# Performance work log

Measured on AMD Instinct MI355X. Metric: run time of the kernel, lower is better.

## Reference

```python
import jax, jax.numpy as jnp
import numpy as np

B, N, F, S = 32, 512, 101, 10   # batch, set size, str_fea_len, expansion_size
E, H, L = 128, 4, 3             # embed_dim, num_heads, n_encoders
EH = E * H
TAB = 100                       # atom-feature table rows


def _ln(x, g, b, eps=1e-5):
    m = jnp.mean(x, -1, keepdims=True)
    v = jnp.var(x, -1, keepdims=True)
    return (x - m) / jnp.sqrt(v + eps) * g + b


def setup_inputs() -> dict:
    key = jax.random.key(0)
    ks = iter(jax.random.split(key, 48))
    nrm = lambda shape: jax.random.normal(next(ks), shape, jnp.float32) * 0.05
    return {
        'str_fea': jax.random.uniform(next(ks), (B, N, F), jnp.float32),
        'comp_fea': jax.random.randint(next(ks), (B, N), 0, TAB),
        'cell_fea': jax.random.normal(next(ks), (B, 6), jnp.float32),
        'af_table': jax.random.uniform(next(ks), (TAB, 92), jnp.float32),
        'comp_w': nrm((92, E)), 'comp_b': jnp.zeros((E,), jnp.float32),
        'emb_w': nrm(((F - 1) * S, E)), 'emb_b': jnp.zeros((E,), jnp.float32),
        'ln_g': jnp.ones((L, E), jnp.float32), 'ln_b': jnp.zeros((L, E), jnp.float32),
        'wq': nrm((L, E, EH)), 'bq': jnp.zeros((L, EH), jnp.float32),
        'wk': nrm((L, E, EH)), 'bk': jnp.zeros((L, EH), jnp.float32),
        'wv': nrm((L, E, EH)), 'bv': jnp.zeros((L, EH), jnp.float32),
        'inproj_w': nrm((L, EH, 3 * EH)), 'inproj_b': jnp.zeros((L, 3 * EH), jnp.float32),
        'out_w': nrm((L, EH, E)), 'out_b': jnp.zeros((L, E), jnp.float32),
        'ffn_w': nrm((L, E, E)), 'ffn_b': jnp.zeros((L, E), jnp.float32),
        'ln2_g': jnp.ones((E,), jnp.float32), 'ln2_b': jnp.zeros((E,), jnp.float32),
        'final_w': nrm((E, 1)), 'final_b': jnp.zeros((1,), jnp.float32),
    }


def reference(str_fea, comp_fea, cell_fea, af_table, comp_w, comp_b, emb_w, emb_b,
              ln_g, ln_b, wq, bq, wk, bk, wv, bv, inproj_w, inproj_b,
              out_w, out_b, ffn_w, ffn_b, ln2_g, ln2_b, final_w, final_b):
    weights = str_fea[:, :, 0:1]                                  # [B,N,1]
    # AtomFeaturizer + composition embedding
    comp = af_table[comp_fea] @ comp_w + comp_b                   # [B,N,E]
    # DistanceExpansion: (1 - (d - i/S))**2 for i in 0..S-1
    d = str_fea[:, :, 1:]                                         # [B,N,F-1]
    starter = jnp.arange(S, dtype=str_fea.dtype) / S
    de = (1.0 - (d[..., None] - starter)) ** 2                    # [B,N,F-1,S]
    de = de.reshape(d.shape[0], d.shape[1], (F - 1) * S)
    strf = de @ emb_w + emb_b                                     # [B,N,E]
    x = comp + strf
    x_init = x
    mask = jnp.sum(weights, -1) == 0.0                            # [B,N] key padding
    w_row = weights[..., 0]                                       # [B,N]
    hd = EH // H
    scale = 1.0 / np.sqrt(hd)
    for l in range(L):
        xn = _ln(x, ln_g[l], ln_b[l])
        qin = xn @ wq[l] + bq[l]                                  # [B,N,EH]
        kin = xn @ wk[l] + bk[l]
        vin = xn @ wv[l] + bv[l]                                  # used as V in manual attention
        # torch.nn.MultiheadAttention in-projection (v-block unused: att_output discarded)
        q = qin @ inproj_w[l][:, :EH] + inproj_b[l][:EH]
        k = kin @ inproj_w[l][:, EH:2 * EH] + inproj_b[l][EH:2 * EH]
        qh = q.reshape(q.shape[0], q.shape[1], H, hd)
        kh = k.reshape(k.shape[0], k.shape[1], H, hd)
        logits = jnp.einsum('bihd,bjhd->bhij', qh, kh) * scale    # [B,H,N,N]
        logits = jnp.where(mask[:, None, None, :], -1e9, logits)
        attn = jnp.mean(jax.nn.softmax(logits, -1), axis=1)       # head-averaged [B,N,N]
        # external edge-weight masking + renormalization
        aw = attn * w_row[:, None, :]
        aw = aw / jnp.sum(aw, -1, keepdims=True)
        att_out = jnp.einsum('bij,bjd->bid', aw, vin)             # [B,N,EH]
        o1 = x + att_out @ out_w[l] + out_b[l]
        o2 = jax.nn.softplus(_ln(o1, ln_g[l], ln_b[l]) @ ffn_w[l] + ffn_b[l])
        x = _ln(o1 + o2, ln_g[l], ln_b[l])
    x = jnp.sum(weights * (x + x_init), axis=1)                   # weighted pool [B,E]
    x = _ln(x, ln2_g, ln2_b)
    return x @ final_w + final_b                                  # [B,1]
```

## Files before the change

### kernel.cpp

```cpp
#include <hip/hip_runtime.h>
#include <math.h>

#define B_ 32
#define N_ 512
#define F_ 101
#define E_ 128
#define H_ 4
#define EH_ 512
#define L_ 3
#define M_ (B_*N_)

typedef __attribute__((ext_vector_type(8))) short s8v;
typedef __attribute__((ext_vector_type(8))) unsigned short us8v;
typedef __attribute__((ext_vector_type(4))) float f4v;
typedef __attribute__((ext_vector_type(4))) unsigned int u4v;

__device__ __forceinline__ unsigned short f2bf(float f){
  unsigned int u = __builtin_bit_cast(unsigned int, f);
  u += 0x7fffu + ((u>>16)&1u);
  return (unsigned short)(u>>16);
}
__device__ __forceinline__ float bf2f(unsigned int h){
  unsigned int u = h<<16; return __builtin_bit_cast(float, u);
}
__device__ __forceinline__ float softplus_f(float v) {
  return fmaxf(v, 0.f) + log1pf(__expf(-fabsf(v)));
}

#define GLOAD16(gp, lp) __builtin_amdgcn_global_load_lds( \
    (__attribute__((address_space(1))) unsigned int*)(gp), \
    (__attribute__((address_space(3))) unsigned int*)(lp), 16, 0, 0)

#define MFMA16(a,b,c) __builtin_amdgcn_mfma_f32_16x16x32_bf16(a,b,c,0,0,0)

__global__ __launch_bounds__(256) void prepA_kernel(
    const float* __restrict__ wq, const float* __restrict__ wk,
    const float* __restrict__ bq, const float* __restrict__ bk,
    const float* __restrict__ inproj_w,
    float* __restrict__ effpart, float* __restrict__ bpart) {
  __shared__ float As[64][132];
  __shared__ float Bs[64][68];
  const int blk = blockIdx.x;
  const int t = threadIdx.x;
  if (blk < 384) {
    const int bx = blk % 48, ks = blk / 48;
    const int lq = bx>>3, nt = bx&7;
    const int l = lq>>1, qk = lq&1;
    const int bn = nt*64;
    const int k0 = ks*64;
    const float* A = (qk ? wk : wq) + (size_t)l*128*512;
    const float* IP = inproj_w + (size_t)l*512*1536 + qk*512 + bn;
    float acc[8][4];
    #pragma unroll
    for (int i=0;i<8;++i)
      #pragma unroll
      for (int j=0;j<4;++j) acc[i][j]=0.f;
    const int r0 = (t&15)*8, c0 = (t>>4)*4;
    {
      int r = t & 127, half = t>>7;
      #pragma unroll
      for (int u=0;u<8;++u){
        float4 a = *(const float4*)(A + (size_t)r*512 + k0 + half*32 + u*4);
        int kk = half*32 + u*4;
        As[kk+0][r]=a.x; As[kk+1][r]=a.y; As[kk+2][r]=a.z; As[kk+3][r]=a.w;
      }
      int kk = t>>2, cb = (t&3)*16;
      #pragma unroll
      for (int u=0;u<4;++u)
        *(float4*)&Bs[kk][cb+u*4] = *(const float4*)(IP + (size_t)(k0+kk)*1536 + cb + u*4);
    }
    __syncthreads();
    for (int k2=0;k2<64;++k2){
      float4 b = *(const float4*)&Bs[k2][c0];
      float4 a0 = *(const float4*)&As[k2][r0];
      float4 a1 = *(const float4*)&As[k2][r0+4];
      float av[8] = {a0.x,a0.y,a0.z,a0.w,a1.x,a1.y,a1.z,a1.w};
      #pragma unroll
      for (int i=0;i<8;++i){
        acc[i][0] += av[i]*b.x; acc[i][1] += av[i]*b.y;
        acc[i][2] += av[i]*b.z; acc[i][3] += av[i]*b.w;
      }
    }
    #pragma unroll
    for (int j=0;j<4;++j){
      float* dst = effpart + (((size_t)ks*48 + bx)*64 + c0 + j)*128 + r0;
      float4 v0 = {acc[0][j], acc[1][j], acc[2][j], acc[3][j]};
      float4 v1 = {acc[4][j], acc[5][j], acc[6][j], acc[7][j]};
      *(float4*)dst = v0;
      *(float4*)(dst+4) = v1;
    }
  } else {
    const int idxb = blk - 384;
    const int lq = idxb>>3, kt = idxb&7;
    const int l = lq>>1, qk = lq&1;
    const float* bv = (qk?bk:bq) + l*512 + kt*64;
    const float* IP = inproj_w + ((size_t)l*512 + kt*64)*1536 + qk*512;
    float a0=0.f, a1=0.f;
    for (int kk=0; kk<64; ++kk){
      float b = bv[kk];
      const float* row = IP + (size_t)kk*1536;
      a0 += b*row[t];
      a1 += b*row[t+256];
    }
    bpart[(lq*8+kt)*512 + t]       = a0;
    bpart[(lq*8+kt)*512 + t + 256] = a1;
  }
}

__global__ __launch_bounds__(256) void prepB_kernel(
    const float* __restrict__ effpart, const float* __restrict__ bpart,
    const float* __restrict__ wv, const float* __restrict__ out_w,
    const float* __restrict__ ffn_w,
    const float* __restrict__ inproj_b, const float* __restrict__ bvv,
    const float* __restrict__ emb_w, const float* __restrict__ comp_w,
    const float* __restrict__ str_fea, const int* __restrict__ comp_fea,
    const float* __restrict__ af_table,
    unsigned short* __restrict__ wqkvT, unsigned short* __restrict__ outT,
    unsigned short* __restrict__ ffnT, float* __restrict__ bqkv,
    unsigned short* __restrict__ WHi, unsigned short* __restrict__ WLo,
    float* __restrict__ Cpart,
    unsigned short* __restrict__ FHi, unsigned short* __restrict__ FLo,
    float* __restrict__ w_row) {
  const int blk = blockIdx.x;
  const int t = threadIdx.x;
  if (blk < 1536) {
    int idx = blk*256 + t;
    int m = idx & 127;
    int n = (idx>>7) & 511;
    int lq = idx >> 16;
    int l = lq>>1, qk = lq&1;
    size_t base = (((size_t)(lq*8 + (n>>6)))*64 + (n&63))*128 + m;
    float v = 0.f;
    #pragma unroll
    for (int ks=0;ks<8;++ks) v += effpart[(size_t)ks*393216 + base];
    wqkvT[((size_t)l*1536 + qk*512 + n)*128 + m] = f2bf(v);
  } else if (blk < 1662) {
    const int b2 = blk - 1536;
    if (b2 < 108) {
      __shared__ float tile[64][65];
      const float* src; unsigned short* dst; int srcld, dstld;
      if (b2 < 48) {
        int lay = b2/16, rem = b2%16, kt = rem>>3, nt = rem&7;
        src = wv + ((size_t)lay*128 + kt*64)*512 + nt*64; srcld = 512;
        dst = wqkvT + ((size_t)lay*1536 + 1024 + nt*64)*128 + kt*64; dstld = 128;
      } else if (b2 < 96) {
        int b3 = b2-48; int lay = b3/16, rem = b3%16, kt = rem>>1, nt = rem&1;
        src = out_w + ((size_t)lay*512 + kt*64)*128 + nt*64; srcld = 128;
        dst = outT + ((size_t)lay*128 + nt*64)*512 + kt*64; dstld = 512;
      } else {
        int b4 = b2-96; int lay = b4/4, rem = b4%4, kt = rem>>1, nt = rem&1;
        src = ffn_w + ((size_t)lay*128 + kt*64)*128 + nt*64; srcld = 128;
        dst = ffnT + ((size_t)lay*128 + nt*64)*128 + kt*64; dstld = 128;
      }
      #pragma unroll
      for (int rp=0; rp<4; ++rp){
        int r = rp*16 + (t>>4), c = (t&15)*4;
        float4 v = *(const float4*)(src + (size_t)r*srcld + c);
        tile[r][c+0]=v.x; tile[r][c+1]=v.y; tile[r][c+2]=v.z; tile[r][c+3]=v.w;
      }
      __syncthreads();
      #pragma unroll
      for (int wp=0; wp<2; ++wp){
        int n = wp*32 + (t>>3), kk = (t&7)*8;
        us8v pk;
        #pragma unroll
        for (int e=0;e<8;++e) pk[e] = f2bf(tile[kk+e][n]);
        *(us8v*)(dst + (size_t)n*dstld + kk) = pk;
      }
    } else {
      int idx = (b2-108)*256 + t;
      if (idx < 4608) {
        int l = idx/1536, n = idx - l*1536;
        float v;
        if (n < 1024) {
          int qk = n>>9, c = n&511;
          v = inproj_b[(size_t)l*1536 + n];
          #pragma unroll
          for (int kt=0;kt<8;++kt) v += bpart[((l*2+qk)*8+kt)*512 + c];
        } else {
          v = bvv[(size_t)l*512 + (n-1024)];
        }
        bqkv[idx] = v;
      }
    }
  } else if (blk < 1674) {
    if (t < 128) {
      int p = blk - 1662, e = t;
      if (p < 10) {
        float Cp = 0.f;
        for (int ff=0; ff<10; ++ff){
          int f = p*10+ff;
          float A=0.f, Bv=0.f;
          #pragma unroll
          for (int s=0;s<10;++s){
            float wvv = emb_w[(size_t)(f*10+s)*128 + e];
            A += wvv; Bv += 0.2f*s*wvv; Cp += 0.01f*(s*s)*wvv;
          }
          int kA = 92+f, kB = 192+f;
          unsigned short hA = f2bf(A);
          WHi[e*320+kA]=hA; WLo[e*320+kA]=f2bf(A - bf2f(hA));
          unsigned short hB = f2bf(Bv);
          WHi[e*320+kB]=hB; WLo[e*320+kB]=f2bf(Bv - bf2f(hB));
        }
        Cpart[p*128+e] = Cp;
      } else if (p == 10) {
        for (int kk=0;kk<92;++kk){
          float v = comp_w[(size_t)kk*128 + e];
          unsigned short h = f2bf(v);
          WHi[e*320+kk]=h; WLo[e*320+kk]=f2bf(v - bf2f(h));
        }
      } else {
        for (int kk=292;kk<320;++kk){ WHi[e*320+kk]=0; WLo[e*320+kk]=0; }
      }
    }
  } else {
    int g = (blk-1674)*256 + t;
    int row = g / 40, seg = g - row*40;
    const float* sr = str_fea + (size_t)row*F_;
    if (seg == 0) w_row[row] = sr[0];
    const float* af = af_table + (size_t)comp_fea[row]*92;
    const int c0 = seg*8;
    us8v hi, lo;
    #pragma unroll
    for (int e=0;e<8;++e){
      int kk = c0+e; float v;
      if (kk < 92) v = af[kk];
      else if (kk < 192) { float u = 1.f - sr[1+kk-92]; v = u*u; }
      else if (kk < 292) v = 1.f - sr[1+kk-192];
      else v = 0.f;
      unsigned short h = f2bf(v);
      hi[e] = h; lo[e] = f2bf(v - bf2f(h));
    }
    *(us8v*)(FHi + (size_t)row*320 + c0) = hi;
    *(us8v*)(FLo + (size_t)row*320 + c0) = lo;
  }
}

__global__ __launch_bounds__(256) void embgemm_kernel(
    const unsigned short* __restrict__ FHi, const unsigned short* __restrict__ FLo,
    const unsigned short* __restrict__ WHi, const unsigned short* __restrict__ WLo,
    const float* __restrict__ Cpart, const float* __restrict__ comp_b,
    const float* __restrict__ emb_b,
    const float* __restrict__ g0, const float* __restrict__ b0,
    float* __restrict__ x, float* __restrict__ x_init,
    unsigned short* __restrict__ xnb) {
  __shared__ unsigned short lds[24576];
  unsigned short* AHi = lds;
  unsigned short* ALo = lds + 4096;
  unsigned short* BHi = lds + 8192;
  unsigned short* BLo = lds + 16384;
  const int bm = blockIdx.x*64;
  const int t = threadIdx.x, w = t>>6, l = t&63;
  f4v acc[8];
  #pragma unroll
  for (int i=0;i<8;++i) acc[i] = (f4v){0.f,0.f,0.f,0.f};
  const int srow = t>>3, sseg = t&7;
  for (int k0=0;k0<320;k0+=64){
    #pragma unroll
    for (int c=0;c<2;++c){
      int row = c*32+srow;
      GLOAD16(FHi + (size_t)(bm+row)*320 + k0 + ((sseg^(row&7))<<3), (char*)AHi + c*4096 + w*1024);
      GLOAD16(FLo + (size_t)(bm+row)*320 + k0 + ((sseg^(row&7))<<3), (char*)ALo + c*4096 + w*1024);
    }
    #pragma unroll
    for (int c=0;c<4;++c){
      int row = c*32+srow;
      GLOAD16(WHi + (size_t)row*320 + k0 + ((sseg^(row&7))<<3), (char*)BHi + c*4096 + w*1024);
      GLOAD16(WLo + (size_t)row*320 + k0 + ((sseg^(row&7))<<3), (char*)BLo + c*4096 + w*1024);
    }
    __syncthreads();
    #pragma unroll
    for (int ks=0;ks<2;++ks){
      int arow = w*16 + (l&15);
      int aswz = ((((l>>4)+ks*4) ^ (arow&7))<<4);
      s8v ah = *(const s8v*)((const char*)AHi + arow*128 + aswz);
      s8v al = *(const s8v*)((const char*)ALo + arow*128 + aswz);
      #pragma unroll
      for (int ct=0;ct<8;++ct){
        int col = ct*16 + (l&15);
        int bswz = ((((l>>4)+ks*4) ^ (col&7))<<4);
        s8v bh = *(const s8v*)((const char*)BHi + col*128 + bswz);
        s8v bl = *(const s8v*)((const char*)BLo + col*128 + bswz);
        acc[ct] = MFMA16(ah, bh, acc[ct]);
        acc[ct] = MFMA16(ah, bl, acc[ct]);
        acc[ct] = MFMA16(al, bh, acc[ct]);
      }
    }
    __syncthreads();
  }
  float vv[8][4], gc[8], bc[8];
  #pragma unroll
  for (int ct=0;ct<8;++ct){
    int c = ct*16 + (l&15);
    float be = comp_b[c] + emb_b[c];
    for (int p=0;p<10;++p) be += Cpart[p*128+c];
    gc[ct] = g0[c]; bc[ct] = b0[c];
    #pragma unroll
    for (int r=0;r<4;++r) vv[ct][r] = acc[ct][r] + be;
  }
  #pragma unroll
  for (int r=0;r<4;++r){
    float s=0.f, sq=0.f;
    #pragma unroll
    for (int ct=0;ct<8;++ct){ s += vv[ct][r]; sq += vv[ct][r]*vv[ct][r]; }
    #pragma unroll
    for (int m=1;m<16;m<<=1){ s += __shfl_xor(s,m,64); sq += __shfl_xor(sq,m,64); }
    float mean = s*(1.f/128.f);
    float rstd = rsqrtf(sq*(1.f/128.f) - mean*mean + 1e-5f);
    int row = bm + w*16 + (l>>4)*4 + r;
    #pragma unroll
    for (int ct=0;ct<8;++ct){
      int c = ct*16 + (l&15);
      float v = vv[ct][r];
      x[(size_t)row*128 + c] = v;
      x_init[(size_t)row*128 + c] = v;
      xnb[(size_t)row*128 + c] = f2bf((v-mean)*rstd*gc[ct] + bc[ct]);
    }
  }
}

template<int RT>
__global__ __launch_bounds__(256) void mgemm_kernel(
    const unsigned short* __restrict__ A,
    const unsigned short* __restrict__ Bt,
    const float* __restrict__ bias,
    unsigned short* __restrict__ Cb,
    unsigned short* __restrict__ vT,
    int K) {
  constexpr int BM = RT*32;
  __shared__ float smem[8192];
  unsigned short* Al = (unsigned short*)smem;
  unsigned short* Bl = Al + BM*64;
  const int bm = blockIdx.x*BM;
  const int bn = blockIdx.y*128;
  const int t = threadIdx.x;
  const int w = t>>6, l = t&63;
  const int wr = w>>1, wc = w&1;
  f4v acc[RT][4];
  #pragma unroll
  for (int i=0;i<RT;++i)
    #pragma unroll
    for (int j=0;j<4;++j) acc[i][j] = (f4v){0.f,0.f,0.f,0.f};
  const int srow = t>>3, sseg = t&7;
  for (int k0 = 0; k0 < K; k0 += 64) {
    #pragma unroll
    for (int c=0;c<BM/32;++c){
      int row = c*32 + srow;
      GLOAD16(A + (size_t)(bm+row)*K + k0 + ((sseg ^ (row&7))<<3),
              (char*)Al + c*4096 + w*1024);
    }
    #pragma unroll
    for (int c=0;c<4;++c){
      int row = c*32 + srow;
      GLOAD16(Bt + (size_t)(bn+row)*K + k0 + ((sseg ^ (row&7))<<3),
              (char*)Bl + c*4096 + w*1024);
    }
    __syncthreads();
    #pragma unroll
    for (int ks=0;ks<2;++ks){
      s8v bf[4];
      #pragma unroll
      for (int ct=0;ct<4;++ct){
        int col = wc*64 + ct*16 + (l&15);
        bf[ct] = *(const s8v*)((const char*)Bl + col*128 + ((((l>>4)+ks*4) ^ (col&7))<<4));
      }
      #pragma unroll
      for (int rt=0;rt<RT;++rt){
        int arow = wr*(RT*16) + rt*16 + (l&15);
        s8v af = *(const s8v*)((const char*)Al + arow*128 + ((((l>>4)+ks*4) ^ (arow&7))<<4));
        #pragma unroll
        for (int ct=0;ct<4;++ct)
          acc[rt][ct] = MFMA16(af, bf[ct], acc[rt][ct]);
      }
    }
    __syncthreads();
  }
  float bia[4];
  #pragma unroll
  for (int ct=0;ct<4;++ct) bia[ct] = bias[bn + wc*64 + ct*16 + (l&15)];
  unsigned short* lds16 = (unsigned short*)smem;
  if (bn < 1024) {
    #pragma unroll
    for (int rt=0;rt<RT;++rt)
      #pragma unroll
      for (int ct=0;ct<4;++ct)
        #pragma unroll
        for (int r=0;r<4;++r){
          int rr = wr*(RT*16) + rt*16 + (l>>4)*4 + r;
          int cc = wc*64 + ct*16 + (l&15);
          lds16[rr*128 + cc] = f2bf(acc[rt][ct][r] + bia[ct]);
        }
    __syncthreads();
    #pragma unroll
    for (int it=0; it<BM/16; ++it){
      int row = it*16 + (t>>4), seg = t&15;
      u4v v = *(const u4v*)(lds16 + row*128 + seg*8);
      *(u4v*)(Cb + (size_t)(bm+row)*1024 + bn + seg*8) = v;
    }
  } else {
    #pragma unroll
    for (int rt=0;rt<RT;++rt)
      #pragma unroll
      for (int ct=0;ct<4;++ct){
        int rbase = bm + wr*(RT*16) + rt*16 + (l>>4)*4;
        int bb = rbase >> 9, nn = rbase & 511;
        int d = bn - 1024 + wc*64 + ct*16 + (l&15);
        unsigned int lo = (unsigned int)f2bf(acc[rt][ct][0] + bia[ct])
                        | ((unsigned int)f2bf(acc[rt][ct][1] + bia[ct])<<16);
        unsigned int hi = (unsigned int)f2bf(acc[rt][ct][2] + bia[ct])
                        | ((unsigned int)f2bf(acc[rt][ct][3] + bia[ct])<<16);
        uint2 pk; pk.x = lo; pk.y = hi;
        *(uint2*)(vT + ((size_t)(bb*512 + d))*512 + nn) = pk;
      }
  }
}

#define STG_KH(dst, hh, j0s) { \
  _Pragma("unroll") \
  for (int c_=0;c_<8;++c_){ \
    int row_ = c_*32 + w*4 + (l>>4); \
    GLOAD16(qkb + (size_t)(b*512 + (j0s) + row_)*1024 + 512 + (hh)*128 + (((l&15) ^ (row_&7))<<3), \
            (dst) + c_*8192 + w*1024); } }

#define STG_VT(dst, j0s) { \
  _Pragma("unroll") \
  for (int c_=0;c_<4;++c_){ \
    int d_ = c_*128 + w*16 + (l>>2); \
    GLOAD16(vT + ((size_t)(b*512 + d_))*512 + (j0s) + (((l&3) ^ ((d_>>1)&3))<<3), \
            (dst) + c_*8192 + w*1024); } }

#define STG_B2(dst, k0s) { \
  _Pragma("unroll") \
  for (int c_=0;c_<4;++c_){ \
    int n_ = c_*32 + w*4 + (l>>4); \
    GLOAD16(outTl + (size_t)n_*512 + (k0s) + (((l&15) ^ (n_&7))<<3), \
            (dst) + (c_*32 + w*4)*256); } }

#define STG_F1() { \
  _Pragma("unroll") \
  for (int c2_=0;c2_<4;++c2_){ \
    int kh_ = c2_>>1, c_ = c2_&1; \
    int n_ = c_*64 + w*8 + (l>>3); \
    GLOAD16(ffnTl + (size_t)n_*128 + kh_*64 + (((l&7) ^ (n_&7))<<3), \
            ffnB + kh_*16384 + (c_*64 + w*8)*128); } }

__global__ __launch_bounds__(512, 2) void attnX_kernel(
    const unsigned short* __restrict__ qkb, const unsigned short* __restrict__ vT,
    const float* __restrict__ w_row,
    const unsigned short* __restrict__ outTl, const float* __restrict__ out_b,
    const unsigned short* __restrict__ ffnTl, const float* __restrict__ ffn_b,
    float* __restrict__ x, unsigned short* __restrict__ xnb,
    const float* __restrict__ g1, const float* __restrict__ b1,
    const float* __restrict__ g2, const float* __restrict__ b2) {
  __shared__ char smem[136704];
  char* const Kt0 = smem;
  char* const Kt1 = smem + 65536;
  char* const cALc = smem;
  unsigned short* const cAL = (unsigned short*)smem;
  char* const VbA = smem + 66560;
  char* const VbB = smem + 99328;
  float* const w_s    = (float*)(smem + 132096);
  float* const Spart  = (float*)(smem + 134144);
  float* const Rpart  = (float*)(smem + 134656);
  float* const rho_l  = (float*)(smem + 135424);
  float* const zinv_l = (float*)(smem + 136448);
  unsigned short* const outL = (unsigned short*)smem;
  char* const BtA = smem + 66560;
  char* const BtB = smem + 99328;
  float* const vst = (float*)(smem + 66560);
  char* const xnl  = smem;
  char* const ffnB = smem + 16384;

  const int id = blockIdx.x;
  const int b  = (id & 7) | ((id >> 6) << 3);
  const int i0 = ((id >> 3) & 7) * 64;
  const int bm = b*512 + i0;
  const int t = threadIdx.x, w = t>>6, l = t&63;
  const int wi = w & 3, wd = w >> 2;
  const int ib = wi*16 + (l>>4)*4;
  const int arow = wi*16 + (l&15);
  const float SC2 = 1.4426950408889634f * 0.088388347648318447f;

  for (int j=t; j<512; j+=512) w_s[j] = w_row[b*512+j];

  float c_[2][8][4];
  #pragma unroll
  for (int tt=0;tt<2;++tt)
    #pragma unroll
    for (int js=0;js<8;++js)
      #pragma unroll
      for (int r=0;r<4;++r) c_[tt][js][r] = 0.f;

  STG_KH(Kt0, 0, 0);
  __syncthreads();

  char* Kc = Kt0; char* Kn = Kt1;
  #pragma unroll 1
  for (int h=0; h<4; ++h){
    s8v qf[4];
    {
      const unsigned short* qbase = qkb + ((size_t)(bm + arow))*1024 + h*128;
      #pragma unroll
      for (int ks=0;ks<4;++ks) qf[ks] = *(const s8v*)(qbase + ks*32 + (l>>4)*8);
    }
    float Ex[2][8][4];
    #pragma unroll
    for (int tt=0; tt<2; ++tt){
      if (tt==0) { STG_KH(Kn, h, 256); }
      else if (h<3) { STG_KH(Kn, h+1, 0); }
      __builtin_amdgcn_s_setprio(1);
      #pragma unroll
      for (int jsub=0;jsub<8;++jsub){
        const int jcol = wd*128 + jsub*16 + (l&15);
        f4v a = (f4v){0.f,0.f,0.f,0.f};
        #pragma unroll
        for (int ks=0;ks<4;++ks){
          int g = ks*4 + (l>>4);
          s8v kf = *(const s8v*)(Kc + jcol*256 + ((g ^ (jcol&7))<<4));
          a = MFMA16(qf[ks], kf, a);
        }
        #pragma unroll
        for (int r=0;r<4;++r) Ex[tt][jsub][r] = exp2f(a[r]*SC2);
      }
      __builtin_amdgcn_s_setprio(0);
      __syncthreads();
      char* tmp = Kc; Kc = Kn; Kn = tmp;
    }
    float sp[4] = {0.f,0.f,0.f,0.f};
    float rp[4] = {0.f,0.f,0.f,0.f};
    #pragma unroll
    for (int tt=0;tt<2;++tt)
      #pragma unroll
      for (int jsub=0;jsub<8;++jsub){
        int jg = tt*256 + wd*128 + jsub*16 + (l&15);
        float wv = w_s[jg];
        float mw = (wv != 0.f) ? 1.f : 0.f;
        #pragma unroll
        for (int r=0;r<4;++r){
          sp[r] += Ex[tt][jsub][r]*mw;
          rp[r] += Ex[tt][jsub][r]*wv;
        }
      }
    #pragma unroll
    for (int r=0;r<4;++r){
      float s = sp[r], rv = rp[r];
      s += __shfl_xor(s,1,64); rv += __shfl_xor(rv,1,64);
      s += __shfl_xor(s,2,64); rv += __shfl_xor(rv,2,64);
      s += __shfl_xor(s,4,64); rv += __shfl_xor(rv,4,64);
      s += __shfl_xor(s,8,64); rv += __shfl_xor(rv,8,64);
      sp[r] = s; rp[r] = rv;
    }
    if ((l&15)==0){
      #pragma unroll
      for (int r=0;r<4;++r){
        Spart[wd*64 + ib + r] = sp[r];
        Rpart[wd*64 + ib + r] = rp[r];
      }
    }
    __syncthreads();
    if (t < 64){
      float S0 = Spart[t] + Spart[64+t];
      float R = Rpart[t] + Rpart[64+t];
      rho_l[h*64+t] = R/S0;
    }
    float siv[4];
    #pragma unroll
    for (int r=0;r<4;++r)
      siv[r] = 1.f/(Spart[ib + r] + Spart[64 + ib + r]);
    #pragma unroll
    for (int tt=0;tt<2;++tt)
      #pragma unroll
      for (int jsub=0;jsub<8;++jsub)
        #pragma unroll
        for (int r=0;r<4;++r)
          c_[tt][jsub][r] += Ex[tt][jsub][r]*siv[r];
  }

  __syncthreads();
  STG_VT(VbA, 0);
  if (t < 64)
    zinv_l[t] = 1.f/(rho_l[t] + rho_l[64+t] + rho_l[128+t] + rho_l[192+t]);
  #pragma unroll
  for (int tt=0;tt<2;++tt)
    #pragma unroll
    for (int jsub=0;jsub<8;++jsub){
      int jg = tt*256 + wd*128 + jsub*16 + (l&15);
      float wv = w_s[jg];
      #pragma unroll
      for (int r=0;r<4;++r)
        cAL[(ib+r)*520 + jg] = f2bf(c_[tt][jsub][r]*wv);
    }
  __syncthreads();
  float zv[4][4];
  #pragma unroll
  for (int ig=0;ig<4;++ig)
    #pragma unroll
    for (int r=0;r<4;++r) zv[ig][r] = zinv_l[ig*16 + (l>>4)*4 + r];

  f4v pacc[4][4];
  #pragma unroll
  for (int ig=0;ig<4;++ig)
    #pragma unroll
    for (int ds=0;ds<4;++ds) pacc[ig][ds] = (f4v){0.f,0.f,0.f,0.f};
  {
    char* Vc = VbA; char* Vn = VbB;
    #pragma unroll 1
    for (int vt=0; vt<16; ++vt){
      if (vt < 15) STG_VT(Vn, (vt+1)*32);
      int kidx = l>>4;
      s8v af[4];
      #pragma unroll
      for (int ig=0;ig<4;++ig)
        af[ig] = *(const s8v*)(cALc + (ig*16 + (l&15))*1040 + vt*64 + (kidx<<4));
      __builtin_amdgcn_s_setprio(1);
      #pragma unroll
      for (int dsub=0;dsub<4;++dsub){
        int d = w*64 + dsub*16 + (l&15);
        s8v vf = *(const s8v*)(Vc + d*64 + ((kidx ^ ((d>>1)&3))<<4));
        #pragma unroll
        for (int ig=0;ig<4;++ig)
          pacc[ig][dsub] = MFMA16(af[ig], vf, pacc[ig][dsub]);
      }
      __builtin_amdgcn_s_setprio(0);
      __syncthreads();
      char* tmp = Vc; Vc = Vn; Vn = tmp;
    }
  }

  #pragma unroll
  for (int ig=0;ig<4;++ig)
    #pragma unroll
    for (int dsub=0;dsub<4;++dsub){
      int d = w*64 + dsub*16 + (l&15);
      #pragma unroll
      for (int r=0;r<4;++r)
        outL[(ig*16 + (l>>4)*4 + r)*520 + d] = f2bf(pacc[ig][dsub][r]*zv[ig][r]);
    }
  STG_B2(BtA, 0);
  __syncthreads();

  f4v acc1[4];
  #pragma unroll
  for (int ct=0;ct<4;++ct) acc1[ct] = (f4v){0.f,0.f,0.f,0.f};
  {
    char* Bc = BtA; char* Bn = BtB;
    #pragma unroll 1
    for (int tt=0; tt<4; ++tt){
      if (tt < 3) STG_B2(Bn, (tt+1)*128);
      __builtin_amdgcn_s_setprio(1);
      #pragma unroll
      for (int ks=0;ks<4;++ks){
        int kidx = (l>>4) + ks*4;
        s8v af = *(const s8v*)((const char*)outL + arow*1040 + tt*256 + (kidx<<4));
        #pragma unroll
        for (int ct=0;ct<4;++ct){
          int n = wd*64 + ct*16 + (l&15);
          s8v bf = *(const s8v*)(Bc + n*256 + ((kidx ^ (n&7))<<4));
          acc1[ct] = MFMA16(af, bf, acc1[ct]);
        }
      }
      __builtin_amdgcn_s_setprio(0);
      __syncthreads();
      char* tmp = Bc; Bc = Bn; Bn = tmp;
    }
  }

  #pragma unroll
  for (int ct=0;ct<4;++ct){
    int cc = wd*64 + ct*16 + (l&15);
    float ob = out_b[cc];
    #pragma unroll
    for (int r=0;r<4;++r){
      int rr = wi*16 + (l>>4)*4 + r;
      vst[rr*128 + cc] = acc1[ct][r] + ob + x[(size_t)(bm+rr)*128 + cc];
    }
  }
  STG_F1();
  __syncthreads();

  {
    const float2 g1v = *(const float2*)(g1 + l*2);
    const float2 b1v = *(const float2*)(b1 + l*2);
    #pragma unroll
    for (int rr=0; rr<8; ++rr){
      int row = w*8 + rr;
      float2 vv = *(const float2*)&vst[row*128 + l*2];
      float s = vv.x+vv.y, sq = vv.x*vv.x + vv.y*vv.y;
      #pragma unroll
      for (int m=1;m<64;m<<=1){ s += __shfl_xor(s,m,64); sq += __shfl_xor(sq,m,64); }
      float mean = s*(1.f/128.f);
      float rstd = rsqrtf(sq*(1.f/128.f) - mean*mean + 1e-5f);
      float xa = (vv.x-mean)*rstd*g1v.x + b1v.x;
      float xb = (vv.y-mean)*rstd*g1v.y + b1v.y;
      int col = l*2;
      int byte = row*256 + (((col>>3) ^ (row&7))<<4) + ((col&7)<<1);
      unsigned int pk = (unsigned int)f2bf(xa) | ((unsigned int)f2bf(xb)<<16);
      *(unsigned int*)(xnl + byte) = pk;
    }
  }
  __syncthreads();

  f4v acc2[4];
  #pragma unroll
  for (int ct=0;ct<4;++ct) acc2[ct] = (f4v){0.f,0.f,0.f,0.f};
  __builtin_amdgcn_s_setprio(1);
  #pragma unroll
  for (int ks2=0;ks2<4;++ks2){
    int kidx2 = (l>>4) + ks2*4;
    s8v af = *(const s8v*)(xnl + arow*256 + ((kidx2 ^ (arow&7))<<4));
    int kh = ks2>>1, ksb = ks2&1;
    int kb = (l>>4) + ksb*4;
    #pragma unroll
    for (int ct=0;ct<4;++ct){
      int n = wd*64 + ct*16 + (l&15);
      s8v bf = *(const s8v*)(ffnB + kh*16384 + n*128 + ((kb ^ (n&7))<<4));
      acc2[ct] = MFMA16(af, bf, acc2[ct]);
    }
  }
  __builtin_amdgcn_s_setprio(0);
  #pragma unroll
  for (int ct=0;ct<4;++ct){
    int cc = wd*64 + ct*16 + (l&15);
    float fb = ffn_b[cc];
    #pragma unroll
    for (int r=0;r<4;++r){
      int rr = wi*16 + (l>>4)*4 + r;
      vst[rr*128 + cc] += softplus_f(acc2[ct][r] + fb);
    }
  }
  __syncthreads();

  {
    const float2 g1v = *(const float2*)(g1 + l*2);
    const float2 b1v = *(const float2*)(b1 + l*2);
    #pragma unroll
    for (int rr=0; rr<8; ++rr){
      int row = w*8 + rr;
      float2 vv = *(const float2*)&vst[row*128 + l*2];
      float s = vv.x+vv.y, sq = vv.x*vv.x + vv.y*vv.y;
      #pragma unroll
      for (int m=1;m<64;m<<=1){ s += __shfl_xor(s,m,64); sq += __shfl_xor(sq,m,64); }
      float mean = s*(1.f/128.f);
      float rstd = rsqrtf(sq*(1.f/128.f) - mean*mean + 1e-5f);
      float xa = (vv.x-mean)*rstd*g1v.x + b1v.x;
      float xb = (vv.y-mean)*rstd*g1v.y + b1v.y;
      float2 xo; xo.x = xa; xo.y = xb;
      *(float2*)(x + (size_t)(bm+row)*128 + l*2) = xo;
      if (g2) {
        float s2 = xa+xb, sq2 = xa*xa + xb*xb;
        #pragma unroll
        for (int m=1;m<64;m<<=1){ s2 += __shfl_xor(s2,m,64); sq2 += __shfl_xor(sq2,m,64); }
        float mean2 = s2*(1.f/128.f);
        float rstd2 = rsqrtf(sq2*(1.f/128.f) - mean2*mean2 + 1e-5f);
        const float2 g2v = *(const float2*)(g2 + l*2);
        const float2 b2v = *(const float2*)(b2 + l*2);
        float ya = (xa-mean2)*rstd2*g2v.x + b2v.x;
        float yb = (xb-mean2)*rstd2*g2v.y + b2v.y;
        unsigned int pk = (unsigned int)f2bf(ya) | ((unsigned int)f2bf(yb)<<16);
        *(unsigned int*)(xnb + (size_t)(bm+row)*128 + l*2) = pk;
      }
    }
  }
}

__global__ __launch_bounds__(256) void poolfinal_kernel(
    const float* __restrict__ x, const float* __restrict__ x_init,
    const float* __restrict__ w_row,
    const float* __restrict__ g, const float* __restrict__ bt,
    const float* __restrict__ fw, const float* __restrict__ fb,
    float* __restrict__ out) {
  __shared__ float red[2][128];
  __shared__ float red2[4];
  __shared__ float red3[2];
  const int b = blockIdx.x;
  const int t = threadIdx.x;
  const int e = t & 127, half = t >> 7;
  float acc = 0.f;
  for (int n = half*256; n < half*256+256; ++n) {
    float w = w_row[(size_t)b*N_ + n];
    size_t o = ((size_t)b*N_ + n)*E_ + e;
    acc += w * (x[o] + x_init[o]);
  }
  red[half][e] = acc;
  __syncthreads();
  float s=0.f, sq=0.f, v=0.f;
  if (t < 128) {
    v = red[0][t] + red[1][t];
    s = v; sq = v*v;
    #pragma unroll
    for (int m = 1; m < 64; m <<= 1) { s += __shfl_xor(s, m, 64); sq += __shfl_xor(sq, m, 64); }
    if ((t&63) == 0) { red2[(t>>6)*2] = s; red2[(t>>6)*2+1] = sq; }
  }
  __syncthreads();
  float p = 0.f;
  if (t < 128) {
    s = red2[0] + red2[2]; sq = red2[1] + red2[3];
    float mean = s*(1.f/E_), var = sq*(1.f/E_) - mean*mean;
    float rstd = rsqrtf(var + 1e-5f);
    float xl = (v - mean)*rstd*g[t] + bt[t];
    p = xl * fw[t];
    #pragma unroll
    for (int m = 1; m < 64; m <<= 1) p += __shfl_xor(p, m, 64);
    if ((t&63) == 0) red3[t>>6] = p;
  }
  __syncthreads();
  if (t == 0) out[b] = red3[0] + red3[1] + fb[0];
}

extern "C" void kernel_launch(void* const* d_in, const int* in_sizes, int n_in,
                              void* d_out, int out_size, void* d_ws, size_t ws_size,
                              hipStream_t stream) {
  (void)in_sizes; (void)n_in; (void)out_size; (void)ws_size;
  const float* str_fea  = (const float*)d_in[0];
  const int*   comp_fea = (const int*)  d_in[1];
  const float* af_table = (const float*)d_in[3];
  const float* comp_w   = (const float*)d_in[4];
  const float* comp_b   = (const float*)d_in[5];
  const float* emb_w    = (const float*)d_in[6];
  const float* emb_b    = (const float*)d_in[7];
  const float* ln_g     = (const float*)d_in[8];
  const float* ln_b     = (const float*)d_in[9];
  const float* wq       = (const float*)d_in[10];
  const float* bq       = (const float*)d_in[11];
  const float* wk       = (const float*)d_in[12];
  const float* bk       = (const float*)d_in[13];
  const float* wv       = (const float*)d_in[14];
  const float* bv       = (const float*)d_in[15];
  const float* inproj_w = (const float*)d_in[16];
  const float* inproj_b = (const float*)d_in[17];
  const float* out_w    = (const float*)d_in[18];
  const float* out_b    = (const float*)d_in[19];
  const float* ffn_w    = (const float*)d_in[20];
  const float* ffn_b    = (const float*)d_in[21];
  const float* ln2_g    = (const float*)d_in[22];
  const float* ln2_b    = (const float*)d_in[23];
  const float* final_w  = (const float*)d_in[24];
  const float* final_b  = (const float*)d_in[25];
  float* out = (float*)d_out;

  float* ws = (float*)d_ws;
  size_t off = 0;
  float* x      = ws + off; off += 2097152;
  float* x_init = ws + off; off += 2097152;
  float* w_row  = ws + off; off += 16384;
  unsigned short* xnb  = (unsigned short*)(ws + off); off += 1048576;
  unsigned short* qkb  = (unsigned short*)(ws + off); off += 8388608;
  unsigned short* vTb  = (unsigned short*)(ws + off); off += 4194304;
  float* bpart  = ws + off; off += 24576;
  float* effpart= ws + off; off += 3145728;
  float* bqkv   = ws + off; off += 4608;
  unsigned short* wqkvT = (unsigned short*)(ws + off); off += 294912;
  unsigned short* outT  = (unsigned short*)(ws + off); off += 98304;
  unsigned short* ffnT  = (unsigned short*)(ws + off); off += 24576;
  unsigned short* FHi   = (unsigned short*)(ws + off); off += 2621440;
  unsigned short* FLo   = (unsigned short*)(ws + off); off += 2621440;
  unsigned short* WHi   = (unsigned short*)(ws + off); off += 20480;
  unsigned short* WLo   = (unsigned short*)(ws + off); off += 20480;
  float* Cpart  = ws + off; off += 1280;

  prepA_kernel<<<432, 256, 0, stream>>>(wq, wk, bq, bk, inproj_w, effpart, bpart);
  prepB_kernel<<<4234, 256, 0, stream>>>(effpart, bpart, wv, out_w, ffn_w,
                                         inproj_b, bv, emb_w, comp_w,
                                         str_fea, comp_fea, af_table,
                                         wqkvT, outT, ffnT, bqkv,
                                         WHi, WLo, Cpart, FHi, FLo, w_row);
  embgemm_kernel<<<M_/64, 256, 0, stream>>>(FHi, FLo, WHi, WLo, Cpart, comp_b, emb_b,
                                            ln_g, ln_b, x, x_init, xnb);

  for (int l = 0; l < L_; ++l) {
    mgemm_kernel<4><<<dim3(M_/128, 12), 256, 0, stream>>>(
        xnb, wqkvT + (size_t)l*196608, bqkv + l*1536, qkb, vTb, 128);
    attnX_kernel<<<256, 512, 0, stream>>>(
        qkb, vTb, w_row,
        outT + (size_t)l*65536, out_b + (size_t)l*E_,
        ffnT + (size_t)l*16384, ffn_b + (size_t)l*E_,
        x, xnb, ln_g + l*E_, ln_b + l*E_,
        (l < 2) ? (ln_g + (l+1)*E_) : nullptr,
        (l < 2) ? (ln_b + (l+1)*E_) : nullptr);
  }

  poolfinal_kernel<<<B_, 256, 0, stream>>>(x, x_init, w_row, ln2_g, ln2_b,
                                           final_w, final_b, out);
}
```

Baseline: 303.7 us.

## Reuse staged A tile across three N tiles in QKV GEMM

The QKV projection GEMM now has each block load its full 128x128 A tile (K=128) into LDS once and loop over three 128-wide output column tiles, staging only the B tile for each. The grid shrinks from 12 to 4 column-blocks, so A is read from global memory a third as often. In exchange each block uses 64KB of LDS, which limits occupancy, and there are fewer blocks in total, with no overlap between B loads and compute.

```diff
diff --git a/kernel.cpp b/kernel.cpp
--- a/kernel.cpp
+++ b/kernel.cpp
@@ -319,99 +319,107 @@
   }
 }
 
-template<int RT>
-__global__ __launch_bounds__(256) void mgemm_kernel(
+__global__ __launch_bounds__(256) void mgemm3_kernel(
     const unsigned short* __restrict__ A,
     const unsigned short* __restrict__ Bt,
     const float* __restrict__ bias,
     unsigned short* __restrict__ Cb,
-    unsigned short* __restrict__ vT,
-    int K) {
-  constexpr int BM = RT*32;
-  __shared__ float smem[8192];
-  unsigned short* Al = (unsigned short*)smem;
-  unsigned short* Bl = Al + BM*64;
-  const int bm = blockIdx.x*BM;
-  const int bn = blockIdx.y*128;
+    unsigned short* __restrict__ vT) {
+  __shared__ char smem[65536];
+  char* const Al = smem;
+  char* const Bl = smem + 32768;
+  unsigned short* const lds16 = (unsigned short*)(smem + 32768);
+  const int bm = blockIdx.x*128;
+  const int bng = blockIdx.y*384;
   const int t = threadIdx.x;
   const int w = t>>6, l = t&63;
   const int wr = w>>1, wc = w&1;
-  f4v acc[RT][4];
-  #pragma unroll
-  for (int i=0;i<RT;++i)
-    #pragma unroll
-    for (int j=0;j<4;++j) acc[i][j] = (f4v){0.f,0.f,0.f,0.f};
   const int srow = t>>3, sseg = t&7;
-  for (int k0 = 0; k0 < K; k0 += 64) {
-    #pragma unroll
-    for (int c=0;c<BM/32;++c){
-      int row = c*32 + srow;
-      GLOAD16(A + (size_t)(bm+row)*K + k0 + ((sseg ^ (row&7))<<3),
-              (char*)Al + c*4096 + w*1024);
-    }
+  #pragma unroll
+  for (int kh=0;kh<2;++kh)
     #pragma unroll
     for (int c=0;c<4;++c){
       int row = c*32 + srow;
-      GLOAD16(Bt + (size_t)(bn+row)*K + k0 + ((sseg ^ (row&7))<<3),
-              (char*)Bl + c*4096 + w*1024);
-    }
+      GLOAD16(A + (size_t)(bm+row)*128 + kh*64 + ((sseg ^ (row&7))<<3),
+              Al + kh*16384 + c*4096 + w*1024);
+    }
+  __syncthreads();
+  #pragma unroll 1
+  for (int nt=0; nt<3; ++nt){
+    const int bn = bng + nt*128;
+    #pragma unroll
+    for (int kh=0;kh<2;++kh)
+      #pragma unroll
+      for (int c=0;c<4;++c){
+        int row = c*32 + srow;
+        GLOAD16(Bt + (size_t)(bn+row)*128 + kh*64 + ((sseg ^ (row&7))<<3),
+                Bl + kh*16384 + c*4096 + w*1024);
+      }
     __syncthreads();
-    #pragma unroll
-    for (int ks=0;ks<2;++ks){
-      s8v bf[4];
-      #pragma unroll
-      for (int ct=0;ct<4;++ct){
-        int col = wc*64 + ct*16 + (l&15);
-        bf[ct] = *(const s8v*)((const char*)Bl + col*128 + ((((l>>4)+ks*4) ^ (col&7))<<4));
-      }
-      #pragma unroll
-      for (int rt=0;rt<RT;++rt){
-        int arow = wr*(RT*16) + rt*16 + (l&15);
-        s8v af = *(const s8v*)((const char*)Al + arow*128 + ((((l>>4)+ks*4) ^ (arow&7))<<4));
+    f4v acc[4][4];
+    #pragma unroll
+    for (int i=0;i<4;++i)
+      #pragma unroll
+      for (int j=0;j<4;++j) acc[i][j] = (f4v){0.f,0.f,0.f,0.f};
+    #pragma unroll
+    for (int kh=0;kh<2;++kh){
+      #pragma unroll
+      for (int ks=0;ks<2;++ks){
+        s8v bf[4];
+        #pragma unroll
+        for (int ct=0;ct<4;++ct){
+          int col = wc*64 + ct*16 + (l&15);
+          bf[ct] = *(const s8v*)(Bl + kh*16384 + col*128 + ((((l>>4)+ks*4) ^ (col&7))<<4));
+        }
+        #pragma unroll
+        for (int rt=0;rt<4;++rt){
+          int arow = wr*64 + rt*16 + (l&15);
+          s8v af = *(const s8v*)(Al + kh*16384 + arow*128 + ((((l>>4)+ks*4) ^ (arow&7))<<4));
+          #pragma unroll
+          for (int ct=0;ct<4;++ct)
+            acc[rt][ct] = MFMA16(af, bf[ct], acc[rt][ct]);
+        }
+      }
+    }
+    __syncthreads();
+    float bia[4];
+    #pragma unroll
+    for (int ct=0;ct<4;++ct) bia[ct] = bias[bn + wc*64 + ct*16 + (l&15)];
+    if (bn < 1024) {
+      #pragma unroll
+      for (int rt=0;rt<4;++rt)
         #pragma unroll
         for (int ct=0;ct<4;++ct)
-          acc[rt][ct] = MFMA16(af, bf[ct], acc[rt][ct]);
-      }
-    }
-    __syncthreads();
-  }
-  float bia[4];
-  #pragma unroll
-  for (int ct=0;ct<4;++ct) bia[ct] = bias[bn + wc*64 + ct*16 + (l&15)];
-  unsigned short* lds16 = (unsigned short*)smem;
-  if (bn < 1024) {
-    #pragma unroll
-    for (int rt=0;rt<RT;++rt)
-      #pragma unroll
-      for (int ct=0;ct<4;++ct)
-        #pragma unroll
-        for (int r=0;r<4;++r){
-          int rr = wr*(RT*16) + rt*16 + (l>>4)*4 + r;
-          int cc = wc*64 + ct*16 + (l&15);
-          lds16[rr*128 + cc] = f2bf(acc[rt][ct][r] + bia[ct]);
+          #pragma unroll
+          for (int r=0;r<4;++r){
+            int rr = wr*64 + rt*16 + (l>>4)*4 + r;
+            int cc = wc*64 + ct*16 + (l&15);
+            lds16[rr*128 + cc] = f2bf(acc[rt][ct][r] + bia[ct]);
+          }
+      __syncthreads();
+      #pragma unroll
+      for (int it=0; it<8; ++it){
+        int row = it*16 + (t>>4), seg = t&15;
+        u4v v = *(const u4v*)(lds16 + row*128 + seg*8);
+        *(u4v*)(Cb + (size_t)(bm+row)*1024 + bn + seg*8) = v;
+      }
+      __syncthreads();
+    } else {
+      #pragma unroll
+      for (int rt=0;rt<4;++rt)
+        #pragma unroll
+        for (int ct=0;ct<4;++ct){
+          int rbase = bm + wr*64 + rt*16 + (l>>4)*4;
+          int bb = rbase >> 9, nn = rbase & 511;
+          int d = bn - 1024 + wc*64 + ct*16 + (l&15);
+          unsigned int lo = (unsigned int)f2bf(acc[rt][ct][0] + bia[ct])
+                          | ((unsigned int)f2bf(acc[rt][ct][1] + bia[ct])<<16);
+          unsigned int hi = (unsigned int)f2bf(acc[rt][ct][2] + bia[ct])
+                          | ((unsigned int)f2bf(acc[rt][ct][3] + bia[ct])<<16);
+          uint2 pk; pk.x = lo; pk.y = hi;
+          *(uint2*)(vT + ((size_t)(bb*512 + d))*512 + nn) = pk;
         }
-    __syncthreads();
-    #pragma unroll
-    for (int it=0; it<BM/16; ++it){
-      int row = it*16 + (t>>4), seg = t&15;
-      u4v v = *(const u4v*)(lds16 + row*128 + seg*8);
-      *(u4v*)(Cb + (size_t)(bm+row)*1024 + bn + seg*8) = v;
-    }
-  } else {
-    #pragma unroll
-    for (int rt=0;rt<RT;++rt)
-      #pragma unroll
-      for (int ct=0;ct<4;++ct){
-        int rbase = bm + wr*(RT*16) + rt*16 + (l>>4)*4;
-        int bb = rbase >> 9, nn = rbase & 511;
-        int d = bn - 1024 + wc*64 + ct*16 + (l&15);
-        unsigned int lo = (unsigned int)f2bf(acc[rt][ct][0] + bia[ct])
-                        | ((unsigned int)f2bf(acc[rt][ct][1] + bia[ct])<<16);
-        unsigned int hi = (unsigned int)f2bf(acc[rt][ct][2] + bia[ct])
-                        | ((unsigned int)f2bf(acc[rt][ct][3] + bia[ct])<<16);
-        uint2 pk; pk.x = lo; pk.y = hi;
-        *(uint2*)(vT + ((size_t)(bb*512 + d))*512 + nn) = pk;
-      }
+    }
   }
 }
 
@@ -868,8 +876,8 @@
                                             ln_g, ln_b, x, x_init, xnb);
 
   for (int l = 0; l < L_; ++l) {
-    mgemm_kernel<4><<<dim3(M_/128, 12), 256, 0, stream>>>(
-        xnb, wqkvT + (size_t)l*196608, bqkv + l*1536, qkb, vTb, 128);
+    mgemm3_kernel<<<dim3(M_/128, 4), 256, 0, stream>>>(
+        xnb, wqkvT + (size_t)l*196608, bqkv + l*1536, qkb, vTb);
     attnX_kernel<<<256, 512, 0, stream>>>(
         qkb, vTb, w_row,
         outT + (size_t)l*65536, out_b + (size_t)l*E_,
```

New measurement: 300.9 us. Within noise of the previous version (-0.9%).
